# Kernel optimization log

Hardware: AMD Instinct MI355X
Metric: run time of the kernel (lower is better)

Reference implementation:

```python
import jax, jax.numpy as jnp
import numpy as np

GRID_SIZE = 5
SPLINE_ORDER = 3
IN_LO, IN_HI = -1.0, 1.0
NOISE_SCALE = 0.1
DENOM_EPS = 1e-8


def setup_inputs() -> dict:
    key = jax.random.key(0)
    k1, k2 = jax.random.split(key)
    x = jax.random.normal(k1, (2048, 4096), dtype=jnp.float32)
    ext = 0.1 * (IN_HI - IN_LO)
    n_knots = GRID_SIZE + 2 * SPLINE_ORDER + 1  # 12
    grid = jnp.linspace(IN_LO - ext, IN_HI + ext, n_knots).astype(jnp.float32)
    coefficients = (jax.random.normal(k2, (GRID_SIZE + SPLINE_ORDER,), dtype=jnp.float32)
                    * NOISE_SCALE)
    return {"x": x, "grid": grid, "coefficients": coefficients}


def _bspline_bases(x, grid, spline_order):
    """Vectorized iterative Cox-de Boor. x: [...], grid: [n_knots].
    Returns [..., n_knots - 1 - spline_order] order-k basis values."""
    xf = x[..., None]  # [..., 1]
    # order 0: half-open indicator [g_i, g_{i+1})  -> [..., n_knots-1]
    B = ((grid[:-1] <= xf) & (xf < grid[1:])).astype(x.dtype)
    for k in range(1, spline_order + 1):
        g_i = grid[: -(k + 1)]   # grid[i]
        g_ik = grid[k:-1]        # grid[i+k]
        g_i1 = grid[1:-k]        # grid[i+1]
        g_ik1 = grid[k + 1:]     # grid[i+k+1]
        d1 = g_ik - g_i
        d2 = g_ik1 - g_i1
        w1 = jnp.where(d1 > DENOM_EPS, (xf - g_i) / jnp.where(d1 > DENOM_EPS, d1, 1.0), 0.0)
        w2 = jnp.where(d2 > DENOM_EPS, (g_ik1 - xf) / jnp.where(d2 > DENOM_EPS, d2, 1.0), 0.0)
        B = w1 * B[..., :-1] + w2 * B[..., 1:]
    return B


def reference(x, grid, coefficients):
    xc = jnp.clip(x, IN_LO, IN_HI)
    B = _bspline_bases(xc, grid, SPLINE_ORDER)  # [..., 8]
    return jnp.einsum('...i,i->...', B, coefficients)
```

## Files before the change

### kernel.cpp

```cpp
#include <hip/hip_runtime.h>


__global__ void __launch_bounds__(256) bspline_act_kernel(
    const float* __restrict__ x,
    const float* __restrict__ grid,
    const float* __restrict__ coeff,
    float* __restrict__ out,
    int n4)
{
    __shared__ float4 table[11];
    __shared__ float s_g0, s_invh;

    const int tid = threadIdx.x;

    if (tid == 0) {
        float g0  = grid[0];
        float g11 = grid[11];
        float h   = (g11 - g0) * (1.0f / 11.0f);
        s_g0   = g0;
        s_invh = 1.0f / h;
    }
    if (tid < 11) {
        const int j = tid;
        float c[4];
#pragma unroll
        for (int m = 0; m < 4; ++m) {
            int idx = j + m - 3;
            c[m] = (idx >= 0 && idx < 8) ? coeff[idx] : 0.0f;
        }
        const float k6 = 1.0f / 6.0f;
        float A = (c[0] + 4.0f * c[1] + c[2]) * k6;
        float B = (3.0f * (c[2] - c[0])) * k6;
        float C = (3.0f * c[0] - 6.0f * c[1] + 3.0f * c[2]) * k6;
        float D = (-c[0] + 3.0f * c[1] - 3.0f * c[2] + c[3]) * k6;
        table[j] = make_float4(A, B, C, D);
    }
    __syncthreads();

    const float g0   = s_g0;
    const float invh = s_invh;

    const float4* __restrict__ x4 = (const float4*)x;
    float4* __restrict__ o4 = (float4*)out;

    const int stride = gridDim.x * blockDim.x;
    for (int i = blockIdx.x * blockDim.x + tid; i < n4; i += stride) {
        float4 v = x4[i];
        float4 r;
        float* vp = &v.x;
        float* rp = &r.x;
#pragma unroll
        for (int e = 0; e < 4; ++e) {
            float xc = fminf(fmaxf(vp[e], -1.0f), 1.0f);
            float t  = (xc - g0) * invh;
            int   j  = (int)t;
            j = j < 0 ? 0 : (j > 10 ? 10 : j);
            float u  = t - (float)j;
            float4 p = table[j];
            rp[e] = ((p.w * u + p.z) * u + p.y) * u + p.x;
        }
        o4[i] = r;
    }
}

extern "C" void kernel_launch(void* const* d_in, const int* in_sizes, int n_in,
                              void* d_out, int out_size, void* d_ws, size_t ws_size,
                              hipStream_t stream) {
    const float* x     = (const float*)d_in[0];
    const float* grid  = (const float*)d_in[1];
    const float* coeff = (const float*)d_in[2];
    float* out = (float*)d_out;

    const int n  = in_sizes[0];
    const int n4 = n >> 2;

    const int block = 256;
    const int blocks = 2048;
    bspline_act_kernel<<<blocks, block, 0, stream>>>(x, grid, coeff, out, n4);
}
```

Measured before the change: 83.62 us.

## Software-pipeline grid-stride loads with nontemporal access and two-deep prefetch

Issues the first two vector loads before the coefficient-table setup and barrier, so memory latency overlaps the table construction. Each iteration prefetches the next two elements before computing the current pair. Loads and stores use nontemporal builtins to bypass cache retention. This raises register use and adds loop-control complexity in exchange for more outstanding memory requests per thread.

```diff
diff --git a/kernel.cpp b/kernel.cpp
--- a/kernel.cpp
+++ b/kernel.cpp
@@ -1,5 +1,30 @@
 #include <hip/hip_runtime.h>
 
+
+typedef float f4 __attribute__((ext_vector_type(4)));
+
+__device__ __forceinline__ float eval1(float xv, float g0, float invh,
+                                       const float4* __restrict__ table)
+{
+    float xc = fminf(fmaxf(xv, -1.0f), 1.0f);
+    float t  = (xc - g0) * invh;
+    int   j  = (int)t;
+    j = j < 0 ? 0 : (j > 10 ? 10 : j);
+    float u  = t - (float)j;
+    float4 p = table[j];
+    return ((p.w * u + p.z) * u + p.y) * u + p.x;
+}
+
+__device__ __forceinline__ f4 eval4(f4 v, float g0, float invh,
+                                    const float4* __restrict__ table)
+{
+    f4 r;
+    r.x = eval1(v.x, g0, invh, table);
+    r.y = eval1(v.y, g0, invh, table);
+    r.z = eval1(v.z, g0, invh, table);
+    r.w = eval1(v.w, g0, invh, table);
+    return r;
+}
 
 __global__ void __launch_bounds__(256) bspline_act_kernel(
     const float* __restrict__ x,
@@ -12,13 +37,25 @@
     __shared__ float s_g0, s_invh;
 
     const int tid = threadIdx.x;
+    const f4* __restrict__ x4 = (const f4*)x;
+    f4* __restrict__ o4 = (f4*)out;
+
+    const int stride = gridDim.x * blockDim.x;
+    const int base   = blockIdx.x * blockDim.x + tid;
+
+    int i0 = base;
+    int i1 = base + stride;
+    bool va = i0 < n4;
+    bool vb = i1 < n4;
+    f4 a = {0.f, 0.f, 0.f, 0.f}, b = {0.f, 0.f, 0.f, 0.f};
+    if (va) a = __builtin_nontemporal_load(&x4[i0]);
+    if (vb) b = __builtin_nontemporal_load(&x4[i1]);
 
     if (tid == 0) {
         float g0  = grid[0];
         float g11 = grid[11];
-        float h   = (g11 - g0) * (1.0f / 11.0f);
         s_g0   = g0;
-        s_invh = 1.0f / h;
+        s_invh = 11.0f / (g11 - g0);
     }
     if (tid < 11) {
         const int j = tid;
@@ -40,26 +77,25 @@
     const float g0   = s_g0;
     const float invh = s_invh;
 
-    const float4* __restrict__ x4 = (const float4*)x;
-    float4* __restrict__ o4 = (float4*)out;
+    while (va) {
+        const int ni0 = i0 + 2 * stride;
+        const int ni1 = i1 + 2 * stride;
+        const bool vna = ni0 < n4;
+        const bool vnb = ni1 < n4;
+        f4 na = {0.f, 0.f, 0.f, 0.f}, nb = {0.f, 0.f, 0.f, 0.f};
+        if (vna) na = __builtin_nontemporal_load(&x4[ni0]);
+        if (vnb) nb = __builtin_nontemporal_load(&x4[ni1]);
 
-    const int stride = gridDim.x * blockDim.x;
-    for (int i = blockIdx.x * blockDim.x + tid; i < n4; i += stride) {
-        float4 v = x4[i];
-        float4 r;
-        float* vp = &v.x;
-        float* rp = &r.x;
-#pragma unroll
-        for (int e = 0; e < 4; ++e) {
-            float xc = fminf(fmaxf(vp[e], -1.0f), 1.0f);
-            float t  = (xc - g0) * invh;
-            int   j  = (int)t;
-            j = j < 0 ? 0 : (j > 10 ? 10 : j);
-            float u  = t - (float)j;
-            float4 p = table[j];
-            rp[e] = ((p.w * u + p.z) * u + p.y) * u + p.x;
+        f4 ra = eval4(a, g0, invh, table);
+        __builtin_nontemporal_store(ra, &o4[i0]);
+        if (vb) {
+            f4 rb = eval4(b, g0, invh, table);
+            __builtin_nontemporal_store(rb, &o4[i1]);
         }
-        o4[i] = r;
+
+        i0 = ni0; i1 = ni1;
+        a = na; b = nb;
+        va = vna; vb = vnb;
     }
 }
 
```

After: 86.95 us. 4.0% more time.
